# Performance work log

Hardware: AMD Instinct MI355X
Metric: run time of the kernel (lower is better)

## Reference

```python
import jax, jax.numpy as jnp
import numpy as np

N_NODES = 50000
N_EDGES = 400000
DIMS = 32
HEADS = 6
FEAT = DIMS * HEADS  # 192
NEG_SLOPE = 0.2  # PyG GATv2Conv default


def glorot(key, shape):
    fan_in, fan_out = shape[0], shape[1]
    lim = jnp.sqrt(6.0 / (fan_in + fan_out))
    return jax.random.uniform(key, shape, jnp.float32, -lim, lim)


def setup_inputs() -> dict:
    key = jax.random.key(0)
    ks = jax.random.split(key, 10)
    x = jax.random.normal(ks[0], (N_NODES, FEAT), jnp.float32)
    edge_index = jax.random.randint(ks[1], (2, N_EDGES), 0, N_NODES, jnp.int32)
    edge_weights = jax.random.uniform(ks[2], (N_EDGES, 1), jnp.float32)
    W_l = glorot(ks[3], (FEAT, FEAT))   # lin_l: in -> heads*out
    b_l = jnp.zeros((FEAT,), jnp.float32)
    W_r = glorot(ks[4], (FEAT, FEAT))   # lin_r (share_weights=False)
    b_r = jnp.zeros((FEAT,), jnp.float32)
    W_edge = glorot(ks[5], (1, FEAT))   # lin_edge: edge_dim=1 -> heads*out, no bias
    att = glorot(ks[6], (HEADS, DIMS))  # attention vector per head
    bias = jnp.zeros((FEAT,), jnp.float32)
    return {"x": x, "edge_index": edge_index, "edge_weights": edge_weights,
            "W_l": W_l, "b_l": b_l, "W_r": W_r, "b_r": b_r,
            "W_edge": W_edge, "att": att, "bias": bias}


def gatv2_res(x, edge_index, edge_weights, W_l, b_l, W_r, b_r, W_edge, att, bias):
    N = x.shape[0]
    H, C = att.shape
    src0, dst0 = edge_index[0], edge_index[1]

    # add_self_loops with fill_value='mean': self-loop attr = mean of edge_attr over incoming edges
    cnt = jax.ops.segment_sum(jnp.ones((edge_weights.shape[0],), x.dtype), dst0, num_segments=N)
    loop_attr = jax.ops.segment_sum(edge_weights, dst0, num_segments=N) / jnp.maximum(cnt, 1.0)[:, None]
    loops = jnp.arange(N, dtype=src0.dtype)
    src = jnp.concatenate([src0, loops])
    dst = jnp.concatenate([dst0, loops])
    e_attr = jnp.concatenate([edge_weights, loop_attr], axis=0)  # [E+N, 1]

    x_l = (x @ W_l + b_l).reshape(N, H, C)  # source transform
    x_r = (x @ W_r + b_r).reshape(N, H, C)  # target transform
    e_emb = (e_attr @ W_edge).reshape(-1, H, C)

    # per-edge GATv2 score
    m = jax.nn.leaky_relu(x_l[src] + x_r[dst] + e_emb, NEG_SLOPE)  # [E+N, H, C]
    alpha = jnp.einsum('ehc,hc->eh', m, att)  # [E+N, H]

    # segment softmax over edges incident to each target node (self-loops guarantee coverage)
    amax = jax.lax.stop_gradient(jax.ops.segment_max(alpha, dst, num_segments=N))
    ex = jnp.exp(alpha - amax[dst])
    denom = jax.ops.segment_sum(ex, dst, num_segments=N)
    a = ex / denom[dst]  # [E+N, H]

    out = jax.ops.segment_sum(x_l[src] * a[..., None], dst, num_segments=N)  # [N, H, C]
    out = out.reshape(N, H * C) + bias

    # ResLayer: residual + ReLU (dropout = identity in eval mode)
    return jax.nn.relu(x + out)


def reference(x, edge_index, edge_weights, W_l, b_l, W_r, b_r, W_edge, att, bias):
    return gatv2_res(x, edge_index, edge_weights, W_l, b_l, W_r, b_r, W_edge, att, bias)
```

## Files before the change

kernel.cpp:

```cpp
#include <hip/hip_runtime.h>
#include <hip/hip_bf16.h>
#include <math.h>

#define N_NODES 50000
#define N_EDGES 400000
#define HEADS 6
#define DIMS 32
#define FEAT 192
#define NEG_SLOPE 0.2f

typedef __attribute__((ext_vector_type(8))) short short8;
typedef __attribute__((ext_vector_type(4))) float f32x4;

__device__ __forceinline__ unsigned short f2bu(float f) {
    __hip_bfloat16 h = __float2bfloat16(f);
    unsigned short u; __builtin_memcpy(&u, &h, 2); return u;
}
__device__ __forceinline__ float bu2f(unsigned short u) {
    return __uint_as_float(((unsigned)u) << 16);
}

#define XL_OFF    0
#define XR_OFF    19200000
#define WT_OFF    38400000
#define BLR_OFF   38547456
#define PAIR_OFF  38548992
#define DEG_OFF   41748992
#define WSUM_OFF  41948992
#define SCAN_OFF  42148992
#define BSUM_OFF  42348992
#define BOFF_OFF  42350016
#define NB_SCAN ((N_NODES + 255) / 256)

__global__ __launch_bounds__(256) void k_count(const int* __restrict__ ei,
                                               const float* __restrict__ ew,
                                               int* __restrict__ deg,
                                               float* __restrict__ wsum,
                                               const float* __restrict__ Wl,
                                               const float* __restrict__ Wr,
                                               const float* __restrict__ bl,
                                               const float* __restrict__ br,
                                               short* __restrict__ Wt,
                                               float* __restrict__ blr) {
    int e = blockIdx.x * blockDim.x + threadIdx.x;
    if (e < N_EDGES) {
        int d = ei[N_EDGES + e];
        atomicAdd(&deg[d], 1);
        unsafeAtomicAdd(&wsum[d], ew[e]);
    }
    if (e < 384 * FEAT) {
        int n = e / FEAT, k = e - n * FEAT;
        float v = (n < FEAT) ? Wl[k * FEAT + n] : Wr[k * FEAT + (n - FEAT)];
        Wt[n * FEAT + k] = (short)f2bu(v);
    }
    if (e < 384) blr[e] = (e < FEAT) ? bl[e] : br[e - FEAT];
}

__global__ __launch_bounds__(256) void k_scan1(const int* __restrict__ deg,
                                               int* __restrict__ scan,
                                               int* __restrict__ bsums) {
    int t = threadIdx.x;
    int i = blockIdx.x * 256 + t;
    int v = (i < N_NODES) ? deg[i] : 0;
    __shared__ int s[256];
    s[t] = v; __syncthreads();
    for (int off = 1; off < 256; off <<= 1) {
        int u = (t >= off) ? s[t - off] : 0;
        __syncthreads();
        s[t] += u;
        __syncthreads();
    }
    if (i < N_NODES) scan[i] = s[t];
    if (t == 255) bsums[blockIdx.x] = s[255];
}

__global__ __launch_bounds__(256) void k_scan2(int* __restrict__ bsums,
                                               int* __restrict__ boffs) {
    int t = threadIdx.x;
    int v = (t < NB_SCAN) ? bsums[t] : 0;
    __shared__ int s[256];
    s[t] = v; __syncthreads();
    for (int off = 1; off < 256; off <<= 1) {
        int u = (t >= off) ? s[t - off] : 0;
        __syncthreads();
        s[t] += u;
        __syncthreads();
    }
    boffs[t] = s[t] - v;
}

#define SCAT_BLOCKS ((N_EDGES + 383) / 384)
#define GEMM_BLOCKS (N_NODES / 16)
#define OSTRIDE 392
#define ASTRIDE 200
__global__ __launch_bounds__(384) void k_scatgemm(const int* __restrict__ ei,
                                                  const float* __restrict__ ew,
                                                  const int* __restrict__ scan,
                                                  const int* __restrict__ boffs,
                                                  int* __restrict__ deg,
                                                  int2* __restrict__ pair,
                                                  const float* __restrict__ x,
                                                  const short* __restrict__ Wt,
                                                  const float* __restrict__ blr,
                                                  unsigned short* __restrict__ xl,
                                                  unsigned short* __restrict__ xr) {
    __shared__ unsigned short sOut[16 * OSTRIDE];
    __shared__ unsigned short sA[16 * ASTRIDE];
    if (blockIdx.x < SCAT_BLOCKS) {
        int e = blockIdx.x * 384 + threadIdx.x;
        if (e < N_EDGES) {
            int d = ei[N_EDGES + e];
            int inclEnd = boffs[d >> 8] + scan[d];
            int old = atomicSub(&deg[d], 1);
            int2 p; p.x = ei[e]; p.y = __float_as_int(ew[e]);
            pair[inclEnd - old] = p;
        }
        return;
    }
    size_t row0 = (size_t)(blockIdx.x - SCAT_BLOCKS) * 16;

    {
        int q = threadIdx.x;
        int row = q / 24, k0 = (q - row * 24) * 8;
        const float* ap = x + (row0 + row) * FEAT + k0;
        float4 v0 = *(const float4*)ap;
        float4 v1 = *(const float4*)(ap + 4);
        unsigned short tmp[8];
        tmp[0] = f2bu(v0.x); tmp[1] = f2bu(v0.y); tmp[2] = f2bu(v0.z); tmp[3] = f2bu(v0.w);
        tmp[4] = f2bu(v1.x); tmp[5] = f2bu(v1.y); tmp[6] = f2bu(v1.z); tmp[7] = f2bu(v1.w);
        int kw = (k0 >> 1) ^ ((row & 7) << 2);
        *(uint4*)&sA[row * ASTRIDE + kw * 2] = *(const uint4*)tmp;
    }
    __syncthreads();

    int wv   = threadIdx.x >> 6;
    int lane = threadIdx.x & 63;
    int m    = lane & 15;
    int kg   = lane >> 4;
    int ncol0 = wv * 64;

    f32x4 acc0 = {0.f,0.f,0.f,0.f}, acc1 = acc0, acc2 = acc0, acc3 = acc0;

#pragma unroll
    for (int ks = 0; ks < 6; ks++) {
        int kb = ks * 32 + kg * 8;
        int kw = (kb >> 1) ^ ((m & 7) << 2);
        short8 af = *(const short8*)&sA[m * ASTRIDE + kw * 2];
        const short* wp = Wt + (size_t)(ncol0 + m) * FEAT + kb;
        short8 b0 = *(const short8*)(wp);
        short8 b1 = *(const short8*)(wp + 16 * FEAT);
        short8 b2 = *(const short8*)(wp + 32 * FEAT);
        short8 b3 = *(const short8*)(wp + 48 * FEAT);
        acc0 = __builtin_amdgcn_mfma_f32_16x16x32_bf16(af, b0, acc0, 0, 0, 0);
        acc1 = __builtin_amdgcn_mfma_f32_16x16x32_bf16(af, b1, acc1, 0, 0, 0);
        acc2 = __builtin_amdgcn_mfma_f32_16x16x32_bf16(af, b2, acc2, 0, 0, 0);
        acc3 = __builtin_amdgcn_mfma_f32_16x16x32_bf16(af, b3, acc3, 0, 0, 0);
    }

    f32x4 accs[4] = {acc0, acc1, acc2, acc3};
#pragma unroll
    for (int t4 = 0; t4 < 4; t4++) {
        int cc = ncol0 + t4 * 16 + m;
        float bv = blr[cc];
#pragma unroll
        for (int r = 0; r < 4; r++) {
            sOut[(kg * 4 + r) * OSTRIDE + cc] = f2bu(accs[t4][r] + bv);
        }
    }
    __syncthreads();
    for (int q = threadIdx.x; q < 768; q += 384) {
        int row = q / 48, p = q - row * 48;
        uint4 v = *(const uint4*)&sOut[row * OSTRIDE + p * 8];
        if (p < 24) *(uint4*)(xl + (row0 + row) * FEAT + p * 8) = v;
        else        *(uint4*)(xr + (row0 + row) * FEAT + (p - 24) * 8) = v;
    }
}

#define NPB 8
#define CEDGE 32
#define RS 100
#define APAD 36
#define ACS 196
__global__ __launch_bounds__(192) void k_node(const float* __restrict__ x,
                                              const float* __restrict__ bias,
                                              const float* __restrict__ att,
                                              const float* __restrict__ We,
                                              const int* __restrict__ scan,
                                              const int* __restrict__ boffs,
                                              const float* __restrict__ wsum,
                                              const int2* __restrict__ pair,
                                              const unsigned short* __restrict__ xl,
                                              const unsigned short* __restrict__ xr,
                                              float* __restrict__ out) {
    __shared__ __align__(16) unsigned int sXL[CEDGE * RS];
    __shared__ __align__(16) unsigned int sXR[NPB * RS];
    __shared__ float sEx[CEDGE * HEADS];
    __shared__ float sExS[NPB * HEADS];
    __shared__ int   sSrc[2][CEDGE];
    __shared__ float sW[2][CEDGE];
    __shared__ int   sDst[2][CEDGE];
    __shared__ int   sStart[NPB + 1];
    __shared__ __align__(16) float sAttP[HEADS * APAD];
    __shared__ __align__(16) float sWeP[HEADS * APAD];
    __shared__ float sDen[NPB * HEADS];

    int t = threadIdx.x;
    int h = t >> 5;
    int lane = t & 63;
    int wv = t >> 6;
    int n0 = blockIdx.x * NPB;

    int gbase = boffs[n0 >> 8] + ((n0 & 255) ? scan[n0 - 1] : 0);
    int n8 = n0 + NPB;
    int gend = (n8 >= N_NODES) ? N_EDGES
             : (boffs[n8 >> 8] + ((n8 & 255) ? scan[n8 - 1] : 0));
    int etot = gend - gbase;
    int c0 = min(etot, CEDGE);

    if (t < c0) { int2 p = pair[gbase + t]; sSrc[0][t] = p.x; sW[0][t] = __int_as_float(p.y); }

    for (int q = t; q < HEADS * APAD; q += 192) {
        int hh = q / APAD, c = q - hh * APAD;
        if (c < 32) { sAttP[q] = att[hh * 32 + c]; sWeP[q] = We[hh * 32 + c]; }
    }
    if (t <= NPB) {
        int n = n0 + t;
        int st;
        if (n >= N_NODES) st = N_EDGES;
        else {
            int b = n >> 8;
            st = boffs[b] + ((n & 255) ? scan[n - 1] : 0);
        }
        sStart[t] = st;
    }
    if (t < NPB) {
        int n = n0 + t;
        int a = boffs[n >> 8] + ((n & 255) ? scan[n - 1] : 0);
        int n1 = n + 1;
        int b = (n1 >= N_NODES) ? N_EDGES
              : (boffs[n1 >> 8] + ((n1 & 255) ? scan[n1 - 1] : 0));
        int lo = a - gbase; if (lo < 0) lo = 0;
        int hi = b - gbase; if (hi > c0) hi = c0;
        for (int q = lo; q < hi; q++) sDst[0][q] = t;
    }
    {
        int nn = t / 24, p = t - nn * 24;
        *(uint4*)&sXR[nn * RS + p * 4] = ((const uint4*)(xr + (size_t)(n0 + nn) * FEAT))[p];
    }
    __syncthreads();

    f32x4 zz = {0.f,0.f,0.f,0.f};
    f32x4 cA0 = zz, cA1 = zz, cB0 = zz, cB1 = zz, dA = zz, dB = zz;
    short8 kOnes;
#pragma unroll
    for (int j = 0; j < 8; j++) kOnes[j] = (short)0x3F80;

    int nnD = t / HEADS, hhD = t - nnD * HEADS;

    int nch = (etot + CEDGE - 1) / CEDGE;
    for (int ci = 0; ci < nch; ci++) {
        int i0 = ci * CEDGE;
        int c  = min(etot - i0, CEDGE);
        int cn = min(etot - i0 - CEDGE, CEDGE);
        int cb = ci & 1, nb = cb ^ 1;

        {
            int nld = c * 24;
#pragma unroll
            for (int s = 0; s < 4; s++) {
                int q = t + s * 192;
                if (q < nld) {
                    int i = q / 24, p = q - i * 24;
                    *(uint4*)&sXL[i * RS + p * 4] =
                        *(const uint4*)(xl + (size_t)sSrc[cb][i] * FEAT + p * 8);
                }
            }
        }
        int2 P;
        if (t < cn) P = pair[gbase + i0 + CEDGE + t];
        if (t < NPB && cn > 0) {
            int lo = sStart[t] - gbase - i0 - CEDGE;     if (lo < 0) lo = 0;
            int hi = sStart[t + 1] - gbase - i0 - CEDGE; if (hi > cn) hi = cn;
            for (int q = lo; q < hi; q++) sDst[nb][q] = t;
        }
        __syncthreads();

        if (t < c * HEADS) {
            int i = t / HEADS, hh = t - i * HEADS;
            int nn = sDst[cb][i];
            float w = sW[cb][i];
            const uint4* pa = (const uint4*)&sXL[i * RS + hh * 16];
            const uint4* pb = (const uint4*)&sXR[nn * RS + hh * 16];
            float alpha = 0.f;
#pragma unroll
            for (int g = 0; g < 4; g++) {
                uint4 a4 = pa[g];
                uint4 b4 = pb[g];
                float4 we0 = *(const float4*)&sWeP[hh * APAD + g * 8];
                float4 we1 = *(const float4*)&sWeP[hh * APAD + g * 8 + 4];
                float4 at0 = *(const float4*)&sAttP[hh * APAD + g * 8];
                float4 at1 = *(const float4*)&sAttP[hh * APAD + g * 8 + 4];
                float wec[8] = {we0.x, we0.y, we0.z, we0.w, we1.x, we1.y, we1.z, we1.w};
                float atc[8] = {at0.x, at0.y, at0.z, at0.w, at1.x, at1.y, at1.z, at1.w};
                unsigned aw[4] = {a4.x, a4.y, a4.z, a4.w};
                unsigned bw[4] = {b4.x, b4.y, b4.z, b4.w};
#pragma unroll
                for (int q = 0; q < 4; q++) {
                    float m0 = bu2f((unsigned short)aw[q]) + bu2f((unsigned short)bw[q]) + w * wec[q * 2];
                    m0 = fmaxf(m0, NEG_SLOPE * m0);
                    alpha += m0 * atc[q * 2];
                    float m1 = bu2f((unsigned short)(aw[q] >> 16)) + bu2f((unsigned short)(bw[q] >> 16)) + w * wec[q * 2 + 1];
                    m1 = fmaxf(m1, NEG_SLOPE * m1);
                    alpha += m1 * atc[q * 2 + 1];
                }
            }
            sEx[t] = __expf(alpha);
        }
        if (t < cn) { sSrc[nb][t] = P.x; sW[nb][t] = __int_as_float(P.y); }
        __syncthreads();

        {
            const unsigned short* xlu = (const unsigned short*)sXL;
            int g8 = (lane >> 4) * 8;
            int r  = lane & 15;
#pragma unroll
            for (int hid = 0; hid < 2; hid++) {
                int hh = wv * 2 + hid;
                short8 aHi, aLo, b0, b1;
#pragma unroll
                for (int j = 0; j < 8; j++) {
                    int i = g8 + j;
                    bool ok = (i < c);
                    float ex = ok ? sEx[i * HEADS + hh] : 0.f;
                    int dd = sDst[cb][i];
                    unsigned short exHi = f2bu(ex);
                    unsigned short exLo = f2bu(ex - bu2f(exHi));
                    bool own = ok && (dd == r);
                    aHi[j] = own ? (short)exHi : (short)0;
                    aLo[j] = own ? (short)exLo : (short)0;
                    int ub = i * (RS * 2) + hh * 32 + r;
                    b0[j] = ok ? (short)xlu[ub] : (short)0;
                    b1[j] = ok ? (short)xlu[ub + 16] : (short)0;
                }
                if (hid == 0) {
                    cA0 = __builtin_amdgcn_mfma_f32_16x16x32_bf16(aHi, b0, cA0, 0, 0, 0);
                    cA0 = __builtin_amdgcn_mfma_f32_16x16x32_bf16(aLo, b0, cA0, 0, 0, 0);
                    cA1 = __builtin_amdgcn_mfma_f32_16x16x32_bf16(aHi, b1, cA1, 0, 0, 0);
                    cA1 = __builtin_amdgcn_mfma_f32_16x16x32_bf16(aLo, b1, cA1, 0, 0, 0);
                    dA  = __builtin_amdgcn_mfma_f32_16x16x32_bf16(aHi, kOnes, dA, 0, 0, 0);
                    dA  = __builtin_amdgcn_mfma_f32_16x16x32_bf16(aLo, kOnes, dA, 0, 0, 0);
                } else {
                    cB0 = __builtin_amdgcn_mfma_f32_16x16x32_bf16(aHi, b0, cB0, 0, 0, 0);
                    cB0 = __builtin_amdgcn_mfma_f32_16x16x32_bf16(aLo, b0, cB0, 0, 0, 0);
                    cB1 = __builtin_amdgcn_mfma_f32_16x16x32_bf16(aHi, b1, cB1, 0, 0, 0);
                    cB1 = __builtin_amdgcn_mfma_f32_16x16x32_bf16(aLo, b1, cB1, 0, 0, 0);
                    dB  = __builtin_amdgcn_mfma_f32_16x16x32_bf16(aHi, kOnes, dB, 0, 0, 0);
                    dB  = __builtin_amdgcn_mfma_f32_16x16x32_bf16(aLo, kOnes, dB, 0, 0, 0);
                }
            }
        }
        __syncthreads();
    }

    {
        float* sAcc = (float*)sXL;
        int rowg = lane >> 4;
        int cc   = lane & 15;
        if (rowg < 2) {
#pragma unroll
            for (int rg = 0; rg < 4; rg++) {
                int nn = rowg * 4 + rg;
                int h0 = wv * 2, h1 = wv * 2 + 1;
                sAcc[nn * ACS + h0 * 32 + cc]      = cA0[rg];
                sAcc[nn * ACS + h0 * 32 + 16 + cc] = cA1[rg];
                sAcc[nn * ACS + h1 * 32 + cc]      = cB0[rg];
                sAcc[nn * ACS + h1 * 32 + 16 + cc] = cB1[rg];
                if (cc == 0) {
                    sDen[nn * HEADS + h0] = dA[rg];
                    sDen[nn * HEADS + h1] = dB[rg];
                }
            }
        }
    }

    if (t < NPB * HEADS) {
        int nn = nnD, hh = hhD;
        int dg = sStart[nn + 1] - sStart[nn];
        float w = wsum[n0 + nn] / fmaxf((float)dg, 1.0f);
        const uint4* pa = (const uint4*)(xl + (size_t)(n0 + nn) * FEAT + hh * 32);
        const uint4* pb = (const uint4*)&sXR[nn * RS + hh * 16];
        float alpha = 0.f;
#pragma unroll
        for (int g = 0; g < 4; g++) {
            uint4 a4 = pa[g];
            uint4 b4 = pb[g];
            float4 we0 = *(const float4*)&sWeP[hh * APAD + g * 8];
            float4 we1 = *(const float4*)&sWeP[hh * APAD + g * 8 + 4];
            float4 at0 = *(const float4*)&sAttP[hh * APAD + g * 8];
            float4 at1 = *(const float4*)&sAttP[hh * APAD + g * 8 + 4];
            float wec[8] = {we0.x, we0.y, we0.z, we0.w, we1.x, we1.y, we1.z, we1.w};
            float atc[8] = {at0.x, at0.y, at0.z, at0.w, at1.x, at1.y, at1.z, at1.w};
            unsigned aw[4] = {a4.x, a4.y, a4.z, a4.w};
            unsigned bw[4] = {b4.x, b4.y, b4.z, b4.w};
#pragma unroll
            for (int q = 0; q < 4; q++) {
                float m0 = bu2f((unsigned short)aw[q]) + bu2f((unsigned short)bw[q]) + w * wec[q * 2];
                m0 = fmaxf(m0, NEG_SLOPE * m0);
                alpha += m0 * atc[q * 2];
                float m1 = bu2f((unsigned short)(aw[q] >> 16)) + bu2f((unsigned short)(bw[q] >> 16)) + w * wec[q * 2 + 1];
                m1 = fmaxf(m1, NEG_SLOPE * m1);
                alpha += m1 * atc[q * 2 + 1];
            }
        }
        sExS[t] = __expf(alpha);
    }
    __syncthreads();

    {
        const float* sAcc = (const float*)sXL;
        float bj = bias[t];
        float accv[NPB];
#pragma unroll
        for (int nn = 0; nn < NPB; nn++) accv[nn] = sAcc[nn * ACS + t];
#pragma unroll
        for (int nn = 0; nn < NPB; nn++) {
            float exS = sExS[nn * HEADS + h];
            size_t off = (size_t)(n0 + nn) * FEAT + t;
            float xsv = bu2f(xl[off]);
            float num = accv[nn] + exS * xsv;
            float dn  = sDen[nn * HEADS + h] + exS;
            float val = x[off] + bj + num / dn;
            out[off] = (val > 0.f) ? val : 0.f;
        }
    }
}

extern "C" void kernel_launch(void* const* d_in, const int* in_sizes, int n_in,
                              void* d_out, int out_size, void* d_ws, size_t ws_size,
                              hipStream_t stream) {
    const float* x    = (const float*)d_in[0];
    const int*   ei   = (const int*)d_in[1];
    const float* ew   = (const float*)d_in[2];
    const float* Wl   = (const float*)d_in[3];
    const float* bl   = (const float*)d_in[4];
    const float* Wr   = (const float*)d_in[5];
    const float* br   = (const float*)d_in[6];
    const float* We   = (const float*)d_in[7];
    const float* att  = (const float*)d_in[8];
    const float* bias = (const float*)d_in[9];
    float* out = (float*)d_out;

    char* ws = (char*)d_ws;
    unsigned short* xl = (unsigned short*)(ws + XL_OFF);
    unsigned short* xr = (unsigned short*)(ws + XR_OFF);
    short* Wt     = (short*)(ws + WT_OFF);
    float* blr    = (float*)(ws + BLR_OFF);
    int2*  pair   = (int2*)(ws + PAIR_OFF);
    int*   deg    = (int*)(ws + DEG_OFF);
    float* wsum   = (float*)(ws + WSUM_OFF);
    int*   scan   = (int*)(ws + SCAN_OFF);
    int*   bsums  = (int*)(ws + BSUM_OFF);
    int*   boffs  = (int*)(ws + BOFF_OFF);

    hipMemsetAsync(ws + DEG_OFF, 0, 2 * N_NODES * sizeof(int), stream);

    k_count<<<(N_EDGES + 255) / 256, 256, 0, stream>>>(ei, ew, deg, wsum, Wl, Wr, bl, br, Wt, blr);
    k_scan1<<<NB_SCAN, 256, 0, stream>>>(deg, scan, bsums);
    k_scan2<<<1, 256, 0, stream>>>(bsums, boffs);

    k_scatgemm<<<SCAT_BLOCKS + GEMM_BLOCKS, 384, 0, stream>>>(ei, ew, scan, boffs, deg,
                                                              pair, x, Wt, blr, xl, xr);

    k_node<<<N_NODES / NPB, 192, 0, stream>>>(x, bias, att, We, scan, boffs, wsum,
                                              pair, xl, xr, out);
}
```

Measured before the change: 312.4 us.

## Compute softmax denominators and edge-weight sums in registers instead of MFMA/atomics

```diff
diff --git a/kernel.cpp b/kernel.cpp
--- a/kernel.cpp
+++ b/kernel.cpp
@@ -26,16 +26,13 @@
 #define BLR_OFF   38547456
 #define PAIR_OFF  38548992
 #define DEG_OFF   41748992
-#define WSUM_OFF  41948992
 #define SCAN_OFF  42148992
 #define BSUM_OFF  42348992
 #define BOFF_OFF  42350016
 #define NB_SCAN ((N_NODES + 255) / 256)
 
 __global__ __launch_bounds__(256) void k_count(const int* __restrict__ ei,
-                                               const float* __restrict__ ew,
                                                int* __restrict__ deg,
-                                               float* __restrict__ wsum,
                                                const float* __restrict__ Wl,
                                                const float* __restrict__ Wr,
                                                const float* __restrict__ bl,
@@ -43,11 +40,7 @@
                                                short* __restrict__ Wt,
                                                float* __restrict__ blr) {
     int e = blockIdx.x * blockDim.x + threadIdx.x;
-    if (e < N_EDGES) {
-        int d = ei[N_EDGES + e];
-        atomicAdd(&deg[d], 1);
-        unsafeAtomicAdd(&wsum[d], ew[e]);
-    }
+    if (e < N_EDGES) atomicAdd(&deg[ei[N_EDGES + e]], 1);
     if (e < 384 * FEAT) {
         int n = e / FEAT, k = e - n * FEAT;
         float v = (n < FEAT) ? Wl[k * FEAT + n] : Wr[k * FEAT + (n - FEAT)];
@@ -181,20 +174,19 @@
 #define RS 100
 #define APAD 36
 #define ACS 196
-__global__ __launch_bounds__(192) void k_node(const float* __restrict__ x,
+__global__ __launch_bounds__(192, 8) void k_node(const float* __restrict__ x,
                                               const float* __restrict__ bias,
                                               const float* __restrict__ att,
                                               const float* __restrict__ We,
                                               const int* __restrict__ scan,
                                               const int* __restrict__ boffs,
-                                              const float* __restrict__ wsum,
                                               const int2* __restrict__ pair,
                                               const unsigned short* __restrict__ xl,
                                               const unsigned short* __restrict__ xr,
                                               float* __restrict__ out) {
     __shared__ __align__(16) unsigned int sXL[CEDGE * RS];
     __shared__ __align__(16) unsigned int sXR[NPB * RS];
-    __shared__ float sEx[CEDGE * HEADS];
+    __shared__ unsigned int sExP[CEDGE * HEADS];
     __shared__ float sExS[NPB * HEADS];
     __shared__ int   sSrc[2][CEDGE];
     __shared__ float sW[2][CEDGE];
@@ -203,6 +195,7 @@
     __shared__ __align__(16) float sAttP[HEADS * APAD];
     __shared__ __align__(16) float sWeP[HEADS * APAD];
     __shared__ float sDen[NPB * HEADS];
+    __shared__ float sWsm[NPB];
 
     int t = threadIdx.x;
     int h = t >> 5;
@@ -250,10 +243,8 @@
     __syncthreads();
 
     f32x4 zz = {0.f,0.f,0.f,0.f};
-    f32x4 cA0 = zz, cA1 = zz, cB0 = zz, cB1 = zz, dA = zz, dB = zz;
-    short8 kOnes;
-#pragma unroll
-    for (int j = 0; j < 8; j++) kOnes[j] = (short)0x3F80;
+    f32x4 cA0 = zz, cA1 = zz, cB0 = zz, cB1 = zz;
+    float denP0 = 0.f, denP1 = 0.f, wsP = 0.f;
 
     int nnD = t / HEADS, hhD = t - nnD * HEADS;
 
@@ -314,7 +305,10 @@
                     alpha += m1 * atc[q * 2 + 1];
                 }
             }
-            sEx[t] = __expf(alpha);
+            float exv = __expf(alpha);
+            unsigned short hi = f2bu(exv);
+            unsigned short lo = f2bu(exv - bu2f(hi));
+            sExP[t] = ((unsigned)lo << 16) | (unsigned)hi;
         }
         if (t < cn) { sSrc[nb][t] = P.x; sW[nb][t] = __int_as_float(P.y); }
         __syncthreads();
@@ -331,13 +325,18 @@
                 for (int j = 0; j < 8; j++) {
                     int i = g8 + j;
                     bool ok = (i < c);
-                    float ex = ok ? sEx[i * HEADS + hh] : 0.f;
+                    unsigned u = sExP[i * HEADS + hh];
                     int dd = sDst[cb][i];
-                    unsigned short exHi = f2bu(ex);
-                    unsigned short exLo = f2bu(ex - bu2f(exHi));
                     bool own = ok && (dd == r);
-                    aHi[j] = own ? (short)exHi : (short)0;
-                    aLo[j] = own ? (short)exLo : (short)0;
+                    aHi[j] = own ? (short)(u & 0xffffu) : (short)0;
+                    aLo[j] = own ? (short)(u >> 16) : (short)0;
+                    float exf = __uint_as_float(u << 16) + __uint_as_float(u & 0xffff0000u);
+                    if (hid == 0) {
+                        denP0 += own ? exf : 0.f;
+                        wsP   += own ? sW[cb][i] : 0.f;
+                    } else {
+                        denP1 += own ? exf : 0.f;
+                    }
                     int ub = i * (RS * 2) + hh * 32 + r;
                     b0[j] = ok ? (short)xlu[ub] : (short)0;
                     b1[j] = ok ? (short)xlu[ub + 16] : (short)0;
@@ -347,20 +346,20 @@
                     cA0 = __builtin_amdgcn_mfma_f32_16x16x32_bf16(aLo, b0, cA0, 0, 0, 0);
                     cA1 = __builtin_amdgcn_mfma_f32_16x16x32_bf16(aHi, b1, cA1, 0, 0, 0);
                     cA1 = __builtin_amdgcn_mfma_f32_16x16x32_bf16(aLo, b1, cA1, 0, 0, 0);
-                    dA  = __builtin_amdgcn_mfma_f32_16x16x32_bf16(aHi, kOnes, dA, 0, 0, 0);
-                    dA  = __builtin_amdgcn_mfma_f32_16x16x32_bf16(aLo, kOnes, dA, 0, 0, 0);
                 } else {
                     cB0 = __builtin_amdgcn_mfma_f32_16x16x32_bf16(aHi, b0, cB0, 0, 0, 0);
                     cB0 = __builtin_amdgcn_mfma_f32_16x16x32_bf16(aLo, b0, cB0, 0, 0, 0);
                     cB1 = __builtin_amdgcn_mfma_f32_16x16x32_bf16(aHi, b1, cB1, 0, 0, 0);
                     cB1 = __builtin_amdgcn_mfma_f32_16x16x32_bf16(aLo, b1, cB1, 0, 0, 0);
-                    dB  = __builtin_amdgcn_mfma_f32_16x16x32_bf16(aHi, kOnes, dB, 0, 0, 0);
-                    dB  = __builtin_amdgcn_mfma_f32_16x16x32_bf16(aLo, kOnes, dB, 0, 0, 0);
                 }
             }
         }
         __syncthreads();
     }
+
+    denP0 += __shfl_xor(denP0, 16, 64); denP0 += __shfl_xor(denP0, 32, 64);
+    denP1 += __shfl_xor(denP1, 16, 64); denP1 += __shfl_xor(denP1, 32, 64);
+    wsP   += __shfl_xor(wsP,   16, 64); wsP   += __shfl_xor(wsP,   32, 64);
 
     {
         float* sAcc = (float*)sXL;
@@ -375,18 +374,19 @@
                 sAcc[nn * ACS + h0 * 32 + 16 + cc] = cA1[rg];
                 sAcc[nn * ACS + h1 * 32 + cc]      = cB0[rg];
                 sAcc[nn * ACS + h1 * 32 + 16 + cc] = cB1[rg];
-                if (cc == 0) {
-                    sDen[nn * HEADS + h0] = dA[rg];
-                    sDen[nn * HEADS + h1] = dB[rg];
-                }
             }
+        }
+        if (lane < 8) {
+            sDen[lane * HEADS + wv * 2]     = denP0;
+            sDen[lane * HEADS + wv * 2 + 1] = denP1;
+            if (wv == 0) sWsm[lane] = wsP;
         }
     }
 
     if (t < NPB * HEADS) {
         int nn = nnD, hh = hhD;
         int dg = sStart[nn + 1] - sStart[nn];
-        float w = wsum[n0 + nn] / fmaxf((float)dg, 1.0f);
+        float w = sWsm[nn] / fmaxf((float)dg, 1.0f);
         const uint4* pa = (const uint4*)(xl + (size_t)(n0 + nn) * FEAT + hh * 32);
         const uint4* pb = (const uint4*)&sXR[nn * RS + hh * 16];
         float alpha = 0.f;
@@ -457,20 +457,19 @@
     float* blr    = (float*)(ws + BLR_OFF);
     int2*  pair   = (int2*)(ws + PAIR_OFF);
     int*   deg    = (int*)(ws + DEG_OFF);
-    float* wsum   = (float*)(ws + WSUM_OFF);
     int*   scan   = (int*)(ws + SCAN_OFF);
     int*   bsums  = (int*)(ws + BSUM_OFF);
     int*   boffs  = (int*)(ws + BOFF_OFF);
 
-    hipMemsetAsync(ws + DEG_OFF, 0, 2 * N_NODES * sizeof(int), stream);
-
-    k_count<<<(N_EDGES + 255) / 256, 256, 0, stream>>>(ei, ew, deg, wsum, Wl, Wr, bl, br, Wt, blr);
+    hipMemsetAsync(ws + DEG_OFF, 0, N_NODES * sizeof(int), stream);
+
+    k_count<<<(N_EDGES + 255) / 256, 256, 0, stream>>>(ei, deg, Wl, Wr, bl, br, Wt, blr);
     k_scan1<<<NB_SCAN, 256, 0, stream>>>(deg, scan, bsums);
     k_scan2<<<1, 256, 0, stream>>>(bsums, boffs);
 
     k_scatgemm<<<SCAT_BLOCKS + GEMM_BLOCKS, 384, 0, stream>>>(ei, ew, scan, boffs, deg,
                                                               pair, x, Wt, blr, xl, xr);
 
-    k_node<<<N_NODES / NPB, 192, 0, stream>>>(x, bias, att, We, scan, boffs, wsum,
+    k_node<<<N_NODES / NPB, 192, 0, stream>>>(x, bias, att, We, scan, boffs,
                                               pair, xl, xr, out);
 }
```

After: 295.0 us. -5.6%, faster.
